# Performance work log

Hardware: AMD Instinct MI355X
Metric: run time of the kernel (lower is better)

Reference implementation:

```python
import jax, jax.numpy as jnp
import numpy as np
from functools import partial
from jax import lax

B, K, CLIP_DIM, SBERT_DIM, D_MODEL, R_RANK, ATTN_DIM, PMAX = 128, 1024, 768, 384, 256, 64, 256, 8
RHO = 0.35

def _normalize(x, axis=-1, eps=1e-12):
    return x / jnp.maximum(jnp.linalg.norm(x, axis=axis, keepdims=True), eps)

def _build_graph():
    rng = np.random.default_rng(0)
    pid = np.zeros((K, PMAX), np.int32)
    pm = np.zeros((K, PMAX), bool)
    for i in range(K - 1):  # node i's parents are in (i, K); root = K-1 has none
        n = int(rng.integers(1, PMAX + 1))
        n = min(n, K - 1 - i)
        cands = rng.choice(np.arange(i + 1, K), size=n, replace=False)
        pid[i, :n] = cands
        pm[i, :n] = True
    order = np.arange(K - 1, -1, -1, dtype=np.int32)  # parents before children
    return jnp.asarray(pid), jnp.asarray(pm), jnp.asarray(order)

def setup_inputs() -> dict:
    key = jax.random.key(0)
    ks = iter(jax.random.split(key, 32))
    r = lambda shape, s=0.02: jax.random.normal(next(ks), shape, jnp.float32) * s
    pid, pm, order = _build_graph()
    return {
        "t_clip": jax.random.normal(next(ks), (B, CLIP_DIM), jnp.float32),
        "v_clip": jax.random.normal(next(ks), (B, CLIP_DIM), jnp.float32),
        "concept_sbert": jax.random.normal(next(ks), (K, SBERT_DIM), jnp.float32),
        "Wt": r((CLIP_DIM, D_MODEL)), "bt": jnp.zeros((D_MODEL,)),
        "Wv": r((CLIP_DIM, D_MODEL)), "bv": jnp.zeros((D_MODEL,)),
        "Wc": r((SBERT_DIM, D_MODEL)), "bc": jnp.zeros((D_MODEL,)),
        "Wp1": r((3 * D_MODEL, 2 * D_MODEL)), "bp1": jnp.zeros((2 * D_MODEL,)),
        "Wp2": r((2 * D_MODEL, D_MODEL)), "bp2": jnp.zeros((D_MODEL,)),
        "Wm1": r((3 * D_MODEL, 2 * D_MODEL)), "bm1": jnp.zeros((2 * D_MODEL,)),
        "Wm2": r((2 * D_MODEL, D_MODEL)), "bm2": jnp.zeros((D_MODEL,)),
        "tau_logits": jnp.zeros((K,)),
        "U": r((D_MODEL, R_RANK)), "V": r((D_MODEL, R_RANK)),
        "Wg1": r((SBERT_DIM, R_RANK)), "bg1": jnp.zeros((R_RANK,)),
        "Wg2": r((R_RANK, R_RANK)), "bg2": jnp.zeros((R_RANK,)),
        "w_out": r((K, R_RANK)), "b_out": jnp.zeros((K,)),
        "concept_q": r((K, ATTN_DIM)),
        "parents_idx": pid, "parents_mask": pm, "order": order,
    }

def _forward(t_clip, v_clip, concept_sbert, Wt, bt, Wv, bv, Wc, bc,
             Wp1, bp1, Wp2, bp2, Wm1, bm1, Wm2, bm2, tau_logits,
             U, V, Wg1, bg1, Wg2, bg2, w_out, b_out, concept_q,
             parents_idx, parents_mask, order):
    gelu = partial(jax.nn.gelu, approximate=False)  # torch nn.GELU default = exact erf
    t = _normalize(t_clip) @ Wt + bt                 # [B, D]
    v = _normalize(v_clip) @ Wv + bv                 # [B, D]
    d = concept_sbert @ Wc + bc                      # [K, D]
    # x = [v, t, d] broadcast to [B, K, 3D]
    x = jnp.concatenate([
        jnp.broadcast_to(v[:, None, :], (t.shape[0], K, D_MODEL)),
        jnp.broadcast_to(t[:, None, :], (t.shape[0], K, D_MODEL)),
        jnp.broadcast_to(d[None, :, :], (t.shape[0], K, D_MODEL)),
    ], axis=-1)
    h_plus = gelu(x @ Wp1 + bp1) @ Wp2 + bp2
    h_minus = gelu(x @ Wm1 + bm1) @ Wm2 + bm2
    tau = jax.nn.sigmoid(tau_logits)[None, :, None]
    h = tau * h_plus + (1.0 - tau) * h_minus         # [B, K, D]
    u = jnp.einsum('bkd,dr->bkr', h, U)
    vv = jnp.einsum('bkd,dr->bkr', h, V)
    g = gelu(concept_sbert @ Wg1 + bg1) @ Wg2 + bg2  # [K, R]
    inter = u * vv * g[None, :, :]
    logits = jnp.einsum('bkr,kr->bk', inter, w_out) + b_out[None, :]
    p = jax.nn.sigmoid(logits)                        # [B, K]
    # --- top-down hierarchical attention + multiplicative aggregation ---
    q = _normalize(concept_q)                         # [K, A]
    def step(p_hat, node):
        par = parents_idx[node]                       # [P] int
        m = parents_mask[node]                        # [P] bool
        scores = jnp.where(m, q[par] @ q[node], -1e9)
        alpha = jax.nn.softmax(scores)                # [P]
        vals = p_hat[:, par]                          # [B, P] gather of parent probs
        prod = jnp.prod(jnp.where(m[None, :], alpha[None, :] * vals, 1.0), axis=-1)
        new = jnp.where(m.any(), RHO * p[:, node] + (1.0 - RHO) * prod, p_hat[:, node])
        return p_hat.at[:, node].set(new), None       # scatter write
    p_hat, _ = lax.scan(step, p, order)
    return p_hat

def reference(t_clip, v_clip, concept_sbert, Wt, bt, Wv, bv, Wc, bc,
              Wp1, bp1, Wp2, bp2, Wm1, bm1, Wm2, bm2, tau_logits,
              U, V, Wg1, bg1, Wg2, bg2, w_out, b_out, concept_q,
              parents_idx, parents_mask, order):
    return _forward(t_clip, v_clip, concept_sbert, Wt, bt, Wv, bv, Wc, bc,
                    Wp1, bp1, Wp2, bp2, Wm1, bm1, Wm2, bm2, tau_logits,
                    U, V, Wg1, bg1, Wg2, bg2, w_out, b_out, concept_q,
                    parents_idx, parents_mask, order)
```

## Files before the change

kernel.cpp:

```cpp
#include <hip/hip_runtime.h>
#include <math.h>

typedef __attribute__((ext_vector_type(8))) short short8;
typedef __attribute__((ext_vector_type(4))) float float4v;
typedef __attribute__((ext_vector_type(2))) float float2v;

struct P {
  const float *t_clip, *v_clip, *sbert;
  const float *Wt, *bt, *Wv, *bv, *Wc, *bc;
  const float *Wp1, *bp1, *Wp2, *bp2, *Wm1, *bm1, *Wm2, *bm2;
  const float *tau_logits, *U, *V, *Wg1, *bg1, *Wg2, *bg2, *w_out, *b_out, *concept_q;
  const int *pid;
  unsigned short *tvbf;
  unsigned short *sbbf;
  unsigned short *wtvB;
  unsigned short *wcB;
  unsigned short *wg1B;
  unsigned short *wg2B;
  unsigned short *w2bf;
  unsigned short *uvB;
  unsigned short *w1upP, *w1upM;
  unsigned short *w1lowP, *w1lowM;
  unsigned short *vtbf;
  unsigned short *dbf;
  unsigned short *ghbf;
  unsigned short *Ctp, *Ctm;
  unsigned short *Wpk, *Wmk;
  float *Ap, *Am;
  float *sBuf, *biasPM, *tau, *gw, *aprod;
  unsigned short *parS;
  int *sorted, *lvlStart, *nlev;
  float *pOut;
};

__device__ __forceinline__ unsigned short bf16ru(float f) {
    unsigned u = __float_as_uint(f);
    u += 0x7fffu + ((u >> 16) & 1u);
    return (unsigned short)(u >> 16);
}

__device__ __forceinline__ void glds16(const void* g, void* l) {
    __builtin_amdgcn_global_load_lds((const __attribute__((address_space(1))) unsigned int*)g,
                                     (__attribute__((address_space(3))) unsigned int*)l, 16, 0, 0);
}

__device__ __forceinline__ unsigned packpair(float2v a, unsigned c) {
    float2v cb;
    cb.x = __uint_as_float(c << 16);
    cb.y = __uint_as_float(c & 0xffff0000u);
    float2v x = a + cb;
    float2v t = x * x;
    float2v i = t * (-0.06649038f) + 0.39894228f;
    float2v p = x * i + 0.5f;
    float2v g = x * p;
    union { float2v f; unsigned u[2]; } gu; gu.f = g;
    return __builtin_amdgcn_perm(gu.u[1], gu.u[0], 0x07060302u);
}


__device__ void bconv_f(const float* __restrict__ srcRow0, unsigned short* __restrict__ dst,
                        int N, int K16, int kbase, char* smc) {
    unsigned short* wl = (unsigned short*)smc;
    int tid = threadIdx.x;
    int tot4 = 4 * N;
    for (int i4 = tid; i4 < tot4; i4 += 256) {
        float4 w = ((const float4*)srcRow0)[i4];
        ushort4 o;
        o.x = bf16ru(w.x); o.y = bf16ru(w.y); o.z = bf16ru(w.z); o.w = bf16ru(w.w);
        *(ushort4*)&wl[i4 * 4] = o;
    }
    __syncthreads();
    for (int i = tid; i < 2 * N; i += 256) {
        int kg = (i >= N) ? 1 : 0;
        int n = i - kg * N;
        int k0 = kbase + kg * 8;
        ushort4 o0, o1;
        o0.x = wl[(kg * 8 + 0) * N + n]; o0.y = wl[(kg * 8 + 1) * N + n];
        o0.z = wl[(kg * 8 + 2) * N + n]; o0.w = wl[(kg * 8 + 3) * N + n];
        o1.x = wl[(kg * 8 + 4) * N + n]; o1.y = wl[(kg * 8 + 5) * N + n];
        o1.z = wl[(kg * 8 + 6) * N + n]; o1.w = wl[(kg * 8 + 7) * N + n];
        size_t off = (size_t)(n >> 4) * K16 + (k0 >> 5) * 512 + ((k0 >> 3) & 3) * 128 + (n & 15) * 8;
        *(ushort4*)&dst[off]     = o0;
        *(ushort4*)&dst[off + 4] = o1;
    }
}

__device__ void aconv_f(const float* __restrict__ src, unsigned short* __restrict__ dst,
                        int r0, int K, int K16) {
    int tid = threadIdx.x;
    int Kq = K >> 2;
    for (int rl = 0; rl < 16; ++rl) {
        int row = r0 + rl;
        for (int i = tid; i < Kq; i += 256) {
            float4 w = ((const float4*)(src + (size_t)row * K))[i];
            ushort4 o;
            o.x = bf16ru(w.x); o.y = bf16ru(w.y); o.z = bf16ru(w.z); o.w = bf16ru(w.w);
            int k4 = i * 4;
            size_t off = (size_t)(row >> 4) * K16 + (k4 >> 5) * 512 + ((k4 >> 3) & 3) * 128
                       + (row & 15) * 8 + (k4 & 7);
            *(ushort4*)&dst[off] = o;
        }
    }
}

__device__ void tcv_f(const P& a, int rel) {
    int sel = rel & 1, r8 = rel >> 1;
    const float* X = sel ? a.t_clip : a.v_clip;
    unsigned short* dst = a.tvbf + sel * 98304;
    int tid = threadIdx.x;
    int rl = tid >> 5, l = tid & 31;
    int b = r8 * 8 + rl;
    const float4* src = (const float4*)(X + (size_t)b * 768);
    float ss = 0.f;
#pragma unroll
    for (int j = 0; j < 6; ++j) {
        int i4 = l + j * 32;
        float4 w = src[i4];
        ss += w.x * w.x + w.y * w.y + w.z * w.z + w.w * w.w;
        ushort4 o;
        o.x = bf16ru(w.x); o.y = bf16ru(w.y); o.z = bf16ru(w.z); o.w = bf16ru(w.w);
        int k4 = i4 * 4;
        size_t off = (size_t)(b >> 4) * 12288 + (k4 >> 5) * 512 + ((k4 >> 3) & 3) * 128
                   + (b & 15) * 8 + (k4 & 7);
        *(ushort4*)&dst[off] = o;
    }
#pragma unroll
    for (int mk = 16; mk; mk >>= 1) ss += __shfl_xor(ss, mk);
    if (l == 0) a.sBuf[sel * 128 + b] = 1.0f / fmaxf(sqrtf(ss), 1e-12f);
}

__device__ void uvconv_f(const P& a, int blk, char* smc) {
    unsigned short* wl = (unsigned short*)smc;
    int kbase = blk * 16;
    int tid = threadIdx.x;
    for (int i = tid; i < 2048; i += 256) {
        int kl = i >> 7, n = i & 127;
        float v = (n < 64) ? a.U[(size_t)(kbase + kl) * 64 + n]
                           : a.V[(size_t)(kbase + kl) * 64 + (n - 64)];
        wl[kl * 128 + n] = bf16ru(v);
    }
    __syncthreads();
    {
        int i = tid;
        int kg = i >> 7, n = i & 127;
        int k0 = kbase + kg * 8;
        ushort4 o0, o1;
        o0.x = wl[(kg * 8 + 0) * 128 + n]; o0.y = wl[(kg * 8 + 1) * 128 + n];
        o0.z = wl[(kg * 8 + 2) * 128 + n]; o0.w = wl[(kg * 8 + 3) * 128 + n];
        o1.x = wl[(kg * 8 + 4) * 128 + n]; o1.y = wl[(kg * 8 + 5) * 128 + n];
        o1.z = wl[(kg * 8 + 6) * 128 + n]; o1.w = wl[(kg * 8 + 7) * 128 + n];
        size_t off = (size_t)(n >> 4) * 4096 + (k0 >> 5) * 512 + ((k0 >> 3) & 3) * 128 + (n & 15) * 8;
        *(ushort4*)&a.uvB[off]     = o0;
        *(ushort4*)&a.uvB[off + 4] = o1;
    }
}

__device__ void biasPM_f(const P& a, int blk) {
    int tid = threadIdx.x;
    int o = blk * 32 + (tid >> 3), e = tid & 7;
    const float* bb = (o < 128) ? a.bp2 : a.bm2;
    int c = o & 127;
    const float* uv = (c < 64) ? (a.U + c) : (a.V + (c - 64));
    float acc = 0.f;
    for (int d = e * 32; d < e * 32 + 32; ++d)
        acc = fmaf(bb[d], uv[(size_t)d * 64], acc);
    acc += __shfl_xor(acc, 1);
    acc += __shfl_xor(acc, 2);
    acc += __shfl_xor(acc, 4);
    if (e == 0) a.biasPM[o] = acc;
}

__device__ void alpha_f(const P& a, int blk) {
    int t = threadIdx.x, wv = t >> 6, lane = t & 63;
    int node = blk * 4 + wv;
    int slot = lane >> 3, e = lane & 7;
    int par = a.pid[node * 8 + slot];
    const float4* qk = (const float4*)(a.concept_q + (size_t)node * 256);
    const float4* qp = (const float4*)(a.concept_q + (size_t)par * 256);
    float dq = 0, np = 0, ns = 0;
#pragma unroll
    for (int i = 0; i < 8; ++i) {
        float4 x = qp[e * 8 + i], y = qk[e * 8 + i];
        dq += x.x * y.x + x.y * y.y + x.z * y.z + x.w * y.w;
        np += x.x * x.x + x.y * x.y + x.z * x.z + x.w * x.w;
        ns += y.x * y.x + y.y * y.y + y.z * y.z + y.w * y.w;
    }
#pragma unroll
    for (int mk = 1; mk <= 4; mk <<= 1) {
        dq += __shfl_xor(dq, mk); np += __shfl_xor(np, mk); ns += __shfl_xor(ns, mk);
    }
    float score = dq / fmaxf(sqrtf(np) * sqrtf(ns), 1e-24f);
    float sc[8]; int pv[8];
#pragma unroll
    for (int s = 0; s < 8; ++s) { sc[s] = __shfl(score, s * 8); pv[s] = __shfl(par, s * 8); }
    float mx = -1e30f;
#pragma unroll
    for (int s = 0; s < 8; ++s) if (pv[s] != 0) mx = fmaxf(mx, sc[s]);
    float sum = 0.f;
#pragma unroll
    for (int s = 0; s < 8; ++s) sum += (pv[s] != 0) ? expf(sc[s] - mx) : 0.0f;
    float ap = 1.0f;
#pragma unroll
    for (int s = 0; s < 8; ++s) if (pv[s] != 0) ap *= expf(sc[s] - mx) / sum;
    if (lane == 0) a.aprod[node] = ap;
    if (e == 0) a.parS[node * 8 + slot] = (par != 0) ? (unsigned short)par : (unsigned short)1024;
}

__device__ void levels_f(const P& a, int* smemI) {
    volatile int* lvl = smemI;
    unsigned short* parL = (unsigned short*)(smemI + 1024);
    int* cnt  = smemI + 1024 + 4096;
    int* ofs  = smemI + 1024 + 4096 + 1024;
    int* ping = smemI + 1024 + 4096 + 2048;
    int* pong = ping + 256;
    int* mflag = pong + 256;
    int t = threadIdx.x;
    for (int i = t; i < 8192; i += 256) parL[i] = (unsigned short)a.pid[i];
    for (int i = t; i < 1024; i += 256) lvl[i] = 0;
    if (t == 0) mflag[1] = 0;
    __syncthreads();
    if (t < 64) {
        for (int c = 15; c >= 0; --c) {
            int n = c * 64 + t;
            ushort4 pA = *(const ushort4*)&parL[n * 8];
            ushort4 pB = *(const ushort4*)&parL[n * 8 + 4];
            for (;;) {
                int mx = -1;
                if (pA.x) mx = max(mx, lvl[pA.x]);
                if (pA.y) mx = max(mx, lvl[pA.y]);
                if (pA.z) mx = max(mx, lvl[pA.z]);
                if (pA.w) mx = max(mx, lvl[pA.w]);
                if (pB.x) mx = max(mx, lvl[pB.x]);
                if (pB.y) mx = max(mx, lvl[pB.y]);
                if (pB.z) mx = max(mx, lvl[pB.z]);
                if (pB.w) mx = max(mx, lvl[pB.w]);
                int nl = mx + 1;
                bool ch = (nl > lvl[n]);
                if (ch) lvl[n] = nl;
                if (__ballot(ch) == 0ULL) break;
            }
        }
    }
    __syncthreads();
    int lm = 0;
    for (int r = 0; r < 4; ++r) lm = max(lm, lvl[t * 4 + r]);
    atomicMax(&mflag[1], lm);
    for (int r = 0; r < 4; ++r) cnt[t * 4 + r] = 0;
    __syncthreads();
    for (int r = 0; r < 4; ++r) atomicAdd(&cnt[lvl[t * 4 + r]], 1);
    __syncthreads();
    int c0 = cnt[t * 4], c1 = cnt[t * 4 + 1], c2 = cnt[t * 4 + 2], c3 = cnt[t * 4 + 3];
    ping[t] = c0 + c1 + c2 + c3;
    __syncthreads();
    int* src = ping; int* dst = pong;
    for (int off = 1; off < 256; off <<= 1) {
        int v = src[t];
        if (t >= off) v += src[t - off];
        dst[t] = v;
        __syncthreads();
        int* tmp = src; src = dst; dst = tmp;
    }
    int excl = (t == 0) ? 0 : src[t - 1];
    ofs[t * 4] = excl; ofs[t * 4 + 1] = excl + c0;
    ofs[t * 4 + 2] = excl + c0 + c1; ofs[t * 4 + 3] = excl + c0 + c1 + c2;
#pragma unroll
    for (int r = 0; r < 4; ++r) a.lvlStart[t * 4 + r] = ofs[t * 4 + r];
    if (t == 0) { a.lvlStart[1024] = 1024; a.nlev[0] = mflag[1] + 1; }
    __syncthreads();
    for (int r = 0; r < 4; ++r) {
        int n = t * 4 + r;
        int pos = atomicAdd(&ofs[lvl[n]], 1);
        a.sorted[pos] = n;
    }
}

__global__ void __launch_bounds__(256) prep0_kernel(P a) {
    __shared__ int smem[7712];
    int bid = blockIdx.x;
    if (bid == 0) { levels_f(a, smem); return; }
    bid -= 1;
    if (bid < 96) {
        int mat = bid & 1, rb = bid >> 1;
        int r0 = rb * 16;
        const float* W1 = mat ? a.Wm1 : a.Wp1;
        if (r0 < 512) bconv_f(W1 + (size_t)r0 * 512, mat ? a.w1upM : a.w1upP, 512, 8192, r0, (char*)smem);
        else          bconv_f(W1 + (size_t)r0 * 512, mat ? a.w1lowM : a.w1lowP, 512, 4096, r0 - 512, (char*)smem);
        return;
    }
    bid -= 96;
    if (bid < 96) {
        int sel = bid & 1, ch = bid >> 1;
        bconv_f((sel ? a.Wt : a.Wv) + (size_t)ch * 16 * 256, a.wtvB + sel * 196608, 256, 12288, ch * 16, (char*)smem);
        return;
    }
    bid -= 96;
    if (bid < 24) { bconv_f(a.Wc + (size_t)bid * 16 * 256, a.wcB, 256, 6144, bid * 16, (char*)smem); return; }
    bid -= 24;
    if (bid < 24) { bconv_f(a.Wg1 + (size_t)bid * 16 * 64, a.wg1B, 64, 6144, bid * 16, (char*)smem); return; }
    bid -= 24;
    if (bid < 4) { bconv_f(a.Wg2 + (size_t)bid * 16 * 64, a.wg2B, 64, 1024, bid * 16, (char*)smem); return; }
    bid -= 4;
    if (bid < 64) {
        int mat = bid & 1, ch = bid >> 1;
        aconv_f(mat ? a.Wm2 : a.Wp2, a.w2bf + mat * 131072, ch * 16, 256, 4096);
        return;
    }
    bid -= 64;
    if (bid < 16) { uvconv_f(a, bid, (char*)smem); return; }
    bid -= 16;
    if (bid < 32) { tcv_f(a, bid); return; }
    bid -= 32;
    if (bid < 64) { aconv_f(a.sbert, a.sbbf, bid * 16, 384, 6144); return; }
    bid -= 64;
    if (bid < 256) { alpha_f(a, bid); return; }
    bid -= 256;
    if (bid < 8) { biasPM_f(a, bid); return; }
    bid -= 8;
    { int k = bid * 256 + threadIdx.x; a.tau[k] = 1.0f / (1.0f + expf(-a.tau_logits[k])); }
}

__device__ __forceinline__ void gemm64(const unsigned short* A, const unsigned short* B,
                                       int K16A, int K16B, int nsteps,
                                       float4v acc[4], int m, int quad) {
    const unsigned short* Ab = A + quad * 128 + m * 8;
    const unsigned short* Bb = B + quad * 128 + m * 8;
    for (int s = 0; s < nsteps; ++s) {
        short8 af = *(const short8*)(Ab + s * 512);
#pragma unroll
        for (int nt = 0; nt < 4; ++nt) {
            short8 bf = *(const short8*)(Bb + (size_t)nt * K16B + s * 512);
            acc[nt] = __builtin_amdgcn_mfma_f32_16x16x32_bf16(af, bf, acc[nt], 0, 0, 0);
        }
    }
}

__global__ void __launch_bounds__(256) prep1_kernel(P a) {
    int bid = blockIdx.x;
    int tid = threadIdx.x;
    int wv = tid >> 6, lane = tid & 63;
    int m = lane & 15, quad = lane >> 4;
    float4v acc[4];
#pragma unroll
    for (int i = 0; i < 4; ++i) acc[i] = (float4v)0.0f;

    if (bid < 16) {
        int sel = bid & 1, mt = (bid >> 1) & 1, ntile = bid >> 2;
        const unsigned short* A = a.tvbf + sel * 98304 + (size_t)(mt * 4 + wv) * 12288;
        const unsigned short* B = a.wtvB + sel * 196608 + (size_t)(ntile * 4) * 12288;
        gemm64(A, B, 12288, 12288, 24, acc, m, quad);
        const float* bias = sel ? a.bt : a.bv;
#pragma unroll
        for (int nt = 0; nt < 4; ++nt) {
            int col = ntile * 64 + nt * 16 + m;
            int vtcol = sel * 256 + col;
            float bb = bias[col];
#pragma unroll
            for (int r = 0; r < 4; ++r) {
                int row = mt * 64 + wv * 16 + quad * 4 + r;
                float val = acc[nt][r] * a.sBuf[sel * 128 + row] + bb;
                size_t off = (size_t)(row >> 4) * 8192 + (vtcol >> 5) * 512
                           + ((vtcol >> 3) & 3) * 128 + (row & 15) * 8 + (vtcol & 7);
                a.vtbf[off] = bf16ru(val);
            }
        }
        return;
    }
    bid -= 16;
    if (bid < 64) {
        int mt = bid & 15, ntile = bid >> 4;
        const unsigned short* A = a.sbbf + (size_t)(mt * 4 + wv) * 6144;
        const unsigned short* B = a.wcB + (size_t)(ntile * 4) * 6144;
        gemm64(A, B, 6144, 6144, 12, acc, m, quad);
#pragma unroll
        for (int nt = 0; nt < 4; ++nt) {
            int col = ntile * 64 + nt * 16 + m;
            float bb = a.bc[col];
#pragma unroll
            for (int r = 0; r < 4; ++r) {
                int row = mt * 64 + wv * 16 + quad * 4 + r;
                size_t off = (size_t)(row >> 4) * 4096 + (col >> 5) * 512
                           + ((col >> 3) & 3) * 128 + (row & 15) * 8 + (col & 7);
                a.dbf[off] = bf16ru(acc[nt][r] + bb);
            }
        }
        return;
    }
    bid -= 64;
    if (bid < 16) {
        int mt = bid;
        const unsigned short* A = a.sbbf + (size_t)(mt * 4 + wv) * 6144;
        gemm64(A, a.wg1B, 6144, 6144, 12, acc, m, quad);
#pragma unroll
        for (int nt = 0; nt < 4; ++nt) {
            int col = nt * 16 + m;
            float bb = a.bg1[col];
#pragma unroll
            for (int r = 0; r < 4; ++r) {
                int row = mt * 64 + wv * 16 + quad * 4 + r;
                float x = acc[nt][r] + bb;
                float g = 0.5f * x * (1.0f + erff(x * 0.7071067811865475f));
                size_t off = (size_t)(row >> 4) * 1024 + (col >> 5) * 512
                           + ((col >> 3) & 3) * 128 + (row & 15) * 8 + (col & 7);
                a.ghbf[off] = bf16ru(g);
            }
        }
        return;
    }
    bid -= 16;
    {
        int mat = bid & 1, mt = (bid >> 1) & 7, ntile = bid >> 4;
        const unsigned short* A = a.w2bf + mat * 131072 + (size_t)(mt * 4 + wv) * 4096;
        const unsigned short* B = a.uvB + (size_t)(ntile * 4) * 4096;
        gemm64(A, B, 4096, 4096, 8, acc, m, quad);
        unsigned short* outP = mat ? a.Wmk : a.Wpk;
#pragma unroll
        for (int nt = 0; nt < 4; ++nt) {
            int c = ntile * 64 + nt * 16 + m;
#pragma unroll
            for (int r = 0; r < 4; ++r) {
                int j = mt * 64 + wv * 16 + quad * 4 + r;
                size_t o = (size_t)(j >> 5) * 4096 + (c >> 4) * 512 + ((j >> 3) & 3) * 128
                         + (c & 15) * 8 + (j & 7);
                outP[o] = bf16ru(acc[nt][r]);
            }
        }
    }
}

__global__ void __launch_bounds__(256) prep2_kernel(P a) {
    int bid = blockIdx.x;
    int tid = threadIdx.x;
    int wv = tid >> 6, lane = tid & 63;
    int m = lane & 15, quad = lane >> 4;
    if (bid < 256) {
        int mat = bid & 1, mt = (bid >> 1) & 15, ntile = bid >> 5;
        const unsigned short* A = a.dbf + (size_t)(mt * 4 + wv) * 4096 + quad * 128 + m * 8;
        const unsigned short* B = (mat ? a.w1lowM : a.w1lowP) + (size_t)quad * 128 + m * 8;
        unsigned short* Ct = mat ? a.Ctm : a.Ctp;
        float4v acc[4];
#pragma unroll
        for (int i = 0; i < 4; ++i) acc[i] = (float4v)0.0f;
        for (int s = 0; s < 8; ++s) {
            short8 af = *(const short8*)(A + s * 512);
#pragma unroll
            for (int nt = 0; nt < 4; ++nt) {
                short8 bf = *(const short8*)(B + (size_t)(ntile * 4 + nt) * 4096 + s * 512);
                acc[nt] = __builtin_amdgcn_mfma_f32_16x16x32_bf16(af, bf, acc[nt], 0, 0, 0);
            }
        }
        int rowg = mt * 4 + wv;
        int rl = quad * 4;
#pragma unroll
        for (int nt = 0; nt < 4; ++nt) {
            int j = ntile * 64 + nt * 16 + m;
            size_t base = (size_t)rowg * 8192 + (j >> 5) * 512 + ((j >> 3) & 3) * 128 + (j & 7);
#pragma unroll
            for (int rr = 0; rr < 4; ++rr)
                Ct[base + (rl + rr) * 8] = bf16ru(acc[nt][rr]);
        }
        return;
    }
    bid -= 256;
    if (bid < 32) {
        int mat = bid & 1, mt = (bid >> 1) & 1, ntile = bid >> 2;
        const unsigned short* A = a.vtbf + (size_t)(mt * 4 + wv) * 8192 + quad * 128 + m * 8;
        const unsigned short* B = (mat ? a.w1upM : a.w1upP) + (size_t)quad * 128 + m * 8;
        const float* bias = mat ? a.bm1 : a.bp1;
        float* out = mat ? a.Am : a.Ap;
        float4v acc[4];
#pragma unroll
        for (int i = 0; i < 4; ++i) acc[i] = (float4v)0.0f;
        for (int s = 0; s < 16; ++s) {
            short8 af = *(const short8*)(A + s * 512);
#pragma unroll
            for (int nt = 0; nt < 4; ++nt) {
                short8 bf = *(const short8*)(B + (size_t)(ntile * 4 + nt) * 8192 + s * 512);
                acc[nt] = __builtin_amdgcn_mfma_f32_16x16x32_bf16(af, bf, acc[nt], 0, 0, 0);
            }
        }
        int b0r = mt * 64 + wv * 16 + quad * 4;
#pragma unroll
        for (int nt = 0; nt < 4; ++nt) {
            int j = ntile * 64 + nt * 16 + m;
            float bb = bias[j];
#pragma unroll
            for (int rr = 0; rr < 4; ++rr)
                out[(size_t)(b0r + rr) * 512 + j] = acc[nt][rr] + bb;
        }
        return;
    }
    bid -= 32;
    {
        int mt = bid;
        const unsigned short* A = a.ghbf + (size_t)(mt * 4 + wv) * 1024 + quad * 128 + m * 8;
        const unsigned short* B = a.wg2B + (size_t)quad * 128 + m * 8;
        float4v acc[4];
#pragma unroll
        for (int i = 0; i < 4; ++i) acc[i] = (float4v)0.0f;
        for (int s = 0; s < 2; ++s) {
            short8 af = *(const short8*)(A + s * 512);
#pragma unroll
            for (int nt = 0; nt < 4; ++nt) {
                short8 bf = *(const short8*)(B + (size_t)nt * 1024 + s * 512);
                acc[nt] = __builtin_amdgcn_mfma_f32_16x16x32_bf16(af, bf, acc[nt], 0, 0, 0);
            }
        }
#pragma unroll
        for (int nt = 0; nt < 4; ++nt) {
            int col = nt * 16 + m;
            float bb = a.bg2[col];
#pragma unroll
            for (int r = 0; r < 4; ++r) {
                int k = mt * 64 + wv * 16 + quad * 4 + r;
                a.gw[(size_t)k * 64 + col] = (acc[nt][r] + bb) * a.w_out[(size_t)k * 64 + col];
            }
        }
    }
}

__global__ void __launch_bounds__(512, 2) main_kernel(P a) {
    __shared__ float apL[4096];
    __shared__ char wbuf[2][16384];
    int tid = threadIdx.x;
    int wv2 = tid >> 6, lane = tid & 63;
    int mat = wv2 >> 2, sub = wv2 & 3;
    int m = lane & 15, quad = lane >> 4;
    int b0 = (blockIdx.x >> 4) * 4;
    int k0 = (blockIdx.x & 15) << 6;

    for (int i = tid; i < 1024; i += 512) {
        int arr = i >> 7, off = i & 127;
        const float* src = ((arr >> 2) ? a.Am : a.Ap) + (size_t)(b0 + (arr & 3)) * 512;
        ((float4*)apL)[i] = ((const float4*)src)[off];
    }

    const char* wg = ((wv2 < 4) ? (const char*)a.Wpk : (const char*)a.Wmk)
                   + (wv2 & 3) * 2048 + lane * 16;
    char* wl0 = &wbuf[0][wv2 * 2048];
    char* wl1 = &wbuf[1][wv2 * 2048];

    const unsigned short* Ct = mat ? a.Ctm : a.Ctp;
    const float* aL = apL + mat * 2048;
    int kt = (k0 >> 4) + sub;
    const char* ctB = (const char*)Ct + (size_t)kt * 16384 + quad * 256 + m * 16;

    float4v acc[4][8];
#pragma unroll
    for (int b = 0; b < 4; ++b)
#pragma unroll
        for (int i = 0; i < 8; ++i) acc[b][i] = (float4v)0.0f;

    glds16(wg, wl0);
    glds16(wg + 1024, wl0 + 1024);
    uint4 crN = *(const uint4*)(ctB);
    __syncthreads();

    for (int n = 0; n < 16; ++n) {
        if (n < 15) {
            char* dst = ((n + 1) & 1) ? wl1 : wl0;
            glds16(wg + (n + 1) * 8192, dst);
            glds16(wg + (n + 1) * 8192 + 1024, dst + 1024);
        }
        uint4 cr = crN;
        if (n < 15) crN = *(const uint4*)(ctB + (n + 1) * 1024);
        union { uint4 u; short8 s; } fa[4];
        const float* aj = aL + n * 32 + quad * 8;
#pragma unroll
        for (int b = 0; b < 4; ++b) {
            float4v x0 = *(const float4v*)(aj + b * 512);
            float4v x1 = *(const float4v*)(aj + b * 512 + 4);
            float2v v;
            v.x = x0[0]; v.y = x0[1]; fa[b].u.x = packpair(v, cr.x);
            v.x = x0[2]; v.y = x0[3]; fa[b].u.y = packpair(v, cr.y);
            v.x = x1[0]; v.y = x1[1]; fa[b].u.z = packpair(v, cr.z);
            v.x = x1[2]; v.y = x1[3]; fa[b].u.w = packpair(v, cr.w);
        }
        const char* wB = &wbuf[n & 1][0] + mat * 8192 + quad * 256 + m * 16;
#pragma unroll
        for (int nt = 0; nt < 8; ++nt) {
            short8 wf = *(const short8*)(wB + nt * 1024);
            acc[0][nt] = __builtin_amdgcn_mfma_f32_16x16x32_bf16(fa[0].s, wf, acc[0][nt], 0, 0, 0);
            acc[1][nt] = __builtin_amdgcn_mfma_f32_16x16x32_bf16(fa[1].s, wf, acc[1][nt], 0, 0, 0);
            acc[2][nt] = __builtin_amdgcn_mfma_f32_16x16x32_bf16(fa[2].s, wf, acc[2][nt], 0, 0, 0);
            acc[3][nt] = __builtin_amdgcn_mfma_f32_16x16x32_bf16(fa[3].s, wf, acc[3][nt], 0, 0, 0);
        }
        __syncthreads();
    }

    float* xbuf = (float*)wbuf;
    int kk[4]; float tv[4];
#pragma unroll
    for (int r = 0; r < 4; ++r) { kk[r] = k0 + sub * 16 + quad * 4 + r; tv[r] = a.tau[kk[r]]; }
    float lsum[4][4] = {};
#pragma unroll
    for (int t4 = 0; t4 < 4; ++t4) {
        __syncthreads();
        if (mat == 1) {
#pragma unroll
            for (int b = 0; b < 4; ++b) {
                int slot = (sub * 4 + b) * 64 + lane;
#pragma unroll
                for (int r = 0; r < 4; ++r) {
                    xbuf[r * 1024 + slot]       = acc[b][t4][r];
                    xbuf[(r + 4) * 1024 + slot] = acc[b][t4 + 4][r];
                }
            }
        }
        __syncthreads();
        if (mat == 0) {
            int cU = t4 * 16 + m, cV = cU + 64;
            float bPu = a.biasPM[cU], bMu = a.biasPM[128 + cU];
            float bPv = a.biasPM[cV], bMv = a.biasPM[128 + cV];
#pragma unroll
            for (int b = 0; b < 4; ++b) {
                int slot = (sub * 4 + b) * 64 + lane;
#pragma unroll
                for (int r = 0; r < 4; ++r) {
                    float g = a.gw[(size_t)kk[r] * 64 + cU];
                    float u  = tv[r] * (acc[b][t4][r] + bPu)
                             + (1.0f - tv[r]) * (xbuf[r * 1024 + slot] + bMu);
                    float vx = tv[r] * (acc[b][t4 + 4][r] + bPv)
                             + (1.0f - tv[r]) * (xbuf[(r + 4) * 1024 + slot] + bMv);
                    lsum[b][r] = fmaf(u * vx, g, lsum[b][r]);
                }
            }
        }
    }
    if (mat == 0) {
#pragma unroll
        for (int r = 0; r < 4; ++r) {
            float bo = a.b_out[kk[r]];
#pragma unroll
            for (int b = 0; b < 4; ++b) {
                float s = lsum[b][r];
                s += __shfl_xor(s, 1); s += __shfl_xor(s, 2); s += __shfl_xor(s, 4); s += __shfl_xor(s, 8);
                if (m == 0)
                    a.pOut[(size_t)(b0 + b) * 1024 + kk[r]] = 1.0f / (1.0f + expf(-(s + bo)));
            }
        }
    }
}

#define PH_STRIDE 1056
__global__ void __launch_bounds__(256) scan_kernel(P a) {
    __shared__ float ph[4 * PH_STRIDE];
    __shared__ float aprodL[1024];
    __shared__ unsigned short parL[8192];
    __shared__ short sortedL[1024];
    __shared__ int lvlStartL[1025];
    int t = threadIdx.x;
    int b0 = blockIdx.x * 4;
    for (int i = t; i < 1024; i += 256) ((uint4*)parL)[i] = ((const uint4*)a.parS)[i];
    for (int i = t; i < 1024; i += 256) {
        aprodL[i] = a.aprod[i];
        sortedL[i] = (short)a.sorted[i];
        lvlStartL[i] = a.lvlStart[i];
    }
    if (t == 0) lvlStartL[1024] = 1024;
    for (int i = t; i < 4096; i += 256) {
        int bb = i >> 10, k = i & 1023;
        ph[bb * PH_STRIDE + k] = a.pOut[(size_t)(b0 + bb) * 1024 + k];
    }
    if (t < 4) ph[t * PH_STRIDE + 1024] = 1.0f;
    __syncthreads();
    int nlev = a.nlev[0];
    int w = t >> 6, lane = t & 63;
    float* myph = ph + w * PH_STRIDE;
    for (int L = 1; L < nlev; ++L) {
        int s0 = lvlStartL[L], s1 = lvlStartL[L + 1];
        for (int i = s0 + lane; i < s1; i += 64) {
            int node = sortedL[i];
            ushort4 pA = *(const ushort4*)&parL[node * 8];
            ushort4 pB = *(const ushort4*)&parL[node * 8 + 4];
            float prod = aprodL[node];
            prod *= myph[pA.x] * myph[pA.y];
            prod *= myph[pA.z] * myph[pA.w];
            prod *= myph[pB.x] * myph[pB.y];
            prod *= myph[pB.z] * myph[pB.w];
            myph[node] = fmaf(0.35f, myph[node], 0.65f * prod);
        }
    }
    __syncthreads();
    for (int i = t; i < 4096; i += 256) {
        int bb = i >> 10, k = i & 1023;
        a.pOut[(size_t)(b0 + bb) * 1024 + k] = ph[bb * PH_STRIDE + k];
    }
}

extern "C" void kernel_launch(void* const* d_in, const int* in_sizes, int n_in,
                              void* d_out, int out_size, void* d_ws, size_t ws_size,
                              hipStream_t stream) {
    P a;
    a.t_clip = (const float*)d_in[0];
    a.v_clip = (const float*)d_in[1];
    a.sbert  = (const float*)d_in[2];
    a.Wt  = (const float*)d_in[3];  a.bt  = (const float*)d_in[4];
    a.Wv  = (const float*)d_in[5];  a.bv  = (const float*)d_in[6];
    a.Wc  = (const float*)d_in[7];  a.bc  = (const float*)d_in[8];
    a.Wp1 = (const float*)d_in[9];  a.bp1 = (const float*)d_in[10];
    a.Wp2 = (const float*)d_in[11]; a.bp2 = (const float*)d_in[12];
    a.Wm1 = (const float*)d_in[13]; a.bm1 = (const float*)d_in[14];
    a.Wm2 = (const float*)d_in[15]; a.bm2 = (const float*)d_in[16];
    a.tau_logits = (const float*)d_in[17];
    a.U   = (const float*)d_in[18]; a.V   = (const float*)d_in[19];
    a.Wg1 = (const float*)d_in[20]; a.bg1 = (const float*)d_in[21];
    a.Wg2 = (const float*)d_in[22]; a.bg2 = (const float*)d_in[23];
    a.w_out = (const float*)d_in[24]; a.b_out = (const float*)d_in[25];
    a.concept_q = (const float*)d_in[26];
    a.pid = (const int*)d_in[27];

    char* w = (char*)d_ws;
    a.Ctp  = (unsigned short*)(w + 0);
    a.Ctm  = (unsigned short*)(w + 1048576);
    a.tvbf = (unsigned short*)(w + 0);
    a.sbbf = (unsigned short*)(w + 393216);
    a.wtvB = (unsigned short*)(w + 1179648);
    a.wcB  = (unsigned short*)(w + 1966080);
    a.w1upP  = (unsigned short*)(w + 2162688);
    a.w1upM  = (unsigned short*)(w + 2686976);
    a.w1lowP = (unsigned short*)(w + 3211264);
    a.w1lowM = (unsigned short*)(w + 3473408);
    a.wg1B   = (unsigned short*)(w + 3735552);
    a.wg2B   = (unsigned short*)(w + 3784704);
    a.w2bf   = (unsigned short*)(w + 3792896);
    a.uvB    = (unsigned short*)(w + 4317184);
    a.vtbf   = (unsigned short*)(w + 4382720);
    a.dbf    = (unsigned short*)(w + 4513792);
    a.ghbf   = (unsigned short*)(w + 5038080);
    a.Wpk    = (unsigned short*)(w + 5169152);
    a.Wmk    = (unsigned short*)(w + 5300224);
    a.Ap     = (float*)(w + 5431296);
    a.Am     = (float*)(w + 5693440);
    a.biasPM = (float*)(w + 5955584);
    a.tau    = (float*)(w + 5956608);
    a.gw     = (float*)(w + 5960704);
    a.sBuf   = (float*)(w + 6222848);
    a.parS   = (unsigned short*)(w + 6223872);
    a.aprod  = (float*)(w + 6240256);
    a.sorted = (int*)(w + 6244352);
    a.lvlStart = (int*)(w + 6248448);
    a.nlev     = (int*)(w + 6252672);
    a.pOut = (float*)d_out;

    prep0_kernel<<<689, 256, 0, stream>>>(a);
    prep1_kernel<<<128, 256, 0, stream>>>(a);
    prep2_kernel<<<304, 256, 0, stream>>>(a);
    main_kernel<<<512, 512, 0, stream>>>(a);
    scan_kernel<<<32, 256, 0, stream>>>(a);
}
```

Before: 246.1 us.

## Merge prep kernels with grid barriers and fold scan into main kernel tail

Fuses the three prep kernels into one persistent launch of 689 blocks separated by atomic grid-wide barriers, and appends the scan stage to main_kernel: the last 32 blocks to arrive at an atomic counter wait for all blocks, then each runs the level-ordered scan for 4 batch rows. This removes three kernel launch boundaries and their drain/fill gaps. It relies on all 689 prep blocks being co-resident, otherwise the barrier deadlocks. It also adds spin-waiting and a memset launch, and the scan tail runs on only 32 blocks while the rest of the grid has exited.

```diff
diff --git a/kernel.cpp b/kernel.cpp
--- a/kernel.cpp
+++ b/kernel.cpp
@@ -44,6 +44,18 @@
                                      (__attribute__((address_space(3))) unsigned int*)l, 16, 0, 0);
 }
 
+__device__ __forceinline__ void gridbar(unsigned* cnt, unsigned nblk) {
+    __threadfence();
+    __syncthreads();
+    if (threadIdx.x == 0) {
+        __hip_atomic_fetch_add(cnt, 1u, __ATOMIC_RELEASE, __HIP_MEMORY_SCOPE_AGENT);
+        while (__hip_atomic_load(cnt, __ATOMIC_ACQUIRE, __HIP_MEMORY_SCOPE_AGENT) < nblk)
+            __builtin_amdgcn_s_sleep(2);
+    }
+    __syncthreads();
+    __threadfence();
+}
+
 __device__ __forceinline__ unsigned packpair(float2v a, unsigned c) {
     float2v cb;
     cb.x = __uint_as_float(c << 16);
@@ -274,9 +286,7 @@
     }
 }
 
-__global__ void __launch_bounds__(256) prep0_kernel(P a) {
-    __shared__ int smem[7712];
-    int bid = blockIdx.x;
+__device__ void prep0_body(const P& a, int bid, int* smem) {
     if (bid == 0) { levels_f(a, smem); return; }
     bid -= 1;
     if (bid < 96) {
@@ -320,7 +330,7 @@
 }
 
 __device__ __forceinline__ void gemm64(const unsigned short* A, const unsigned short* B,
-                                       int K16A, int K16B, int nsteps,
+                                       int K16B, int nsteps,
                                        float4v acc[4], int m, int quad) {
     const unsigned short* Ab = A + quad * 128 + m * 8;
     const unsigned short* Bb = B + quad * 128 + m * 8;
@@ -334,8 +344,7 @@
     }
 }
 
-__global__ void __launch_bounds__(256) prep1_kernel(P a) {
-    int bid = blockIdx.x;
+__device__ void prep1_body(const P& a, int bid) {
     int tid = threadIdx.x;
     int wv = tid >> 6, lane = tid & 63;
     int m = lane & 15, quad = lane >> 4;
@@ -347,7 +356,7 @@
         int sel = bid & 1, mt = (bid >> 1) & 1, ntile = bid >> 2;
         const unsigned short* A = a.tvbf + sel * 98304 + (size_t)(mt * 4 + wv) * 12288;
         const unsigned short* B = a.wtvB + sel * 196608 + (size_t)(ntile * 4) * 12288;
-        gemm64(A, B, 12288, 12288, 24, acc, m, quad);
+        gemm64(A, B, 12288, 24, acc, m, quad);
         const float* bias = sel ? a.bt : a.bv;
 #pragma unroll
         for (int nt = 0; nt < 4; ++nt) {
@@ -370,7 +379,7 @@
         int mt = bid & 15, ntile = bid >> 4;
         const unsigned short* A = a.sbbf + (size_t)(mt * 4 + wv) * 6144;
         const unsigned short* B = a.wcB + (size_t)(ntile * 4) * 6144;
-        gemm64(A, B, 6144, 6144, 12, acc, m, quad);
+        gemm64(A, B, 6144, 12, acc, m, quad);
 #pragma unroll
         for (int nt = 0; nt < 4; ++nt) {
             int col = ntile * 64 + nt * 16 + m;
@@ -389,7 +398,7 @@
     if (bid < 16) {
         int mt = bid;
         const unsigned short* A = a.sbbf + (size_t)(mt * 4 + wv) * 6144;
-        gemm64(A, a.wg1B, 6144, 6144, 12, acc, m, quad);
+        gemm64(A, a.wg1B, 6144, 12, acc, m, quad);
 #pragma unroll
         for (int nt = 0; nt < 4; ++nt) {
             int col = nt * 16 + m;
@@ -411,7 +420,7 @@
         int mat = bid & 1, mt = (bid >> 1) & 7, ntile = bid >> 4;
         const unsigned short* A = a.w2bf + mat * 131072 + (size_t)(mt * 4 + wv) * 4096;
         const unsigned short* B = a.uvB + (size_t)(ntile * 4) * 4096;
-        gemm64(A, B, 4096, 4096, 8, acc, m, quad);
+        gemm64(A, B, 4096, 8, acc, m, quad);
         unsigned short* outP = mat ? a.Wmk : a.Wpk;
 #pragma unroll
         for (int nt = 0; nt < 4; ++nt) {
@@ -427,8 +436,7 @@
     }
 }
 
-__global__ void __launch_bounds__(256) prep2_kernel(P a) {
-    int bid = blockIdx.x;
+__device__ void prep2_body(const P& a, int bid) {
     int tid = threadIdx.x;
     int wv = tid >> 6, lane = tid & 63;
     int m = lane & 15, quad = lane >> 4;
@@ -518,9 +526,20 @@
     }
 }
 
-__global__ void __launch_bounds__(512, 2) main_kernel(P a) {
-    __shared__ float apL[4096];
-    __shared__ char wbuf[2][16384];
+__global__ void __launch_bounds__(256, 4) prep_all_kernel(P a, unsigned* bar) {
+    __shared__ int smem[7712];
+    prep0_body(a, blockIdx.x, smem);
+    gridbar(&bar[0], 689u);
+    if (blockIdx.x < 128) prep1_body(a, blockIdx.x);
+    gridbar(&bar[1], 689u);
+    if (blockIdx.x < 304) prep2_body(a, blockIdx.x);
+}
+
+__global__ void __launch_bounds__(512, 2) main_kernel(P a, unsigned* barM) {
+    __shared__ char shm[49152];
+    __shared__ unsigned arrivalS;
+    float* apL = (float*)shm;
+    char* wbufB = shm + 16384;
     int tid = threadIdx.x;
     int wv2 = tid >> 6, lane = tid & 63;
     int mat = wv2 >> 2, sub = wv2 & 3;
@@ -536,8 +555,8 @@
 
     const char* wg = ((wv2 < 4) ? (const char*)a.Wpk : (const char*)a.Wmk)
                    + (wv2 & 3) * 2048 + lane * 16;
-    char* wl0 = &wbuf[0][wv2 * 2048];
-    char* wl1 = &wbuf[1][wv2 * 2048];
+    char* wl0 = wbufB + wv2 * 2048;
+    char* wl1 = wbufB + 16384 + wv2 * 2048;
 
     const unsigned short* Ct = mat ? a.Ctm : a.Ctp;
     const float* aL = apL + mat * 2048;
@@ -575,7 +594,7 @@
             v.x = x1[0]; v.y = x1[1]; fa[b].u.z = packpair(v, cr.z);
             v.x = x1[2]; v.y = x1[3]; fa[b].u.w = packpair(v, cr.w);
         }
-        const char* wB = &wbuf[n & 1][0] + mat * 8192 + quad * 256 + m * 16;
+        const char* wB = wbufB + (n & 1) * 16384 + mat * 8192 + quad * 256 + m * 16;
 #pragma unroll
         for (int nt = 0; nt < 8; ++nt) {
             short8 wf = *(const short8*)(wB + nt * 1024);
@@ -587,7 +606,7 @@
         __syncthreads();
     }
 
-    float* xbuf = (float*)wbuf;
+    float* xbuf = (float*)wbufB;
     int kk[4]; float tv[4];
 #pragma unroll
     for (int r = 0; r < 4; ++r) { kk[r] = k0 + sub * 16 + quad * 4 + r; tv[r] = a.tau[kk[r]]; }
@@ -639,51 +658,65 @@
             }
         }
     }
-}
-
-#define PH_STRIDE 1056
-__global__ void __launch_bounds__(256) scan_kernel(P a) {
-    __shared__ float ph[4 * PH_STRIDE];
-    __shared__ float aprodL[1024];
-    __shared__ unsigned short parL[8192];
-    __shared__ short sortedL[1024];
-    __shared__ int lvlStartL[1025];
-    int t = threadIdx.x;
-    int b0 = blockIdx.x * 4;
-    for (int i = t; i < 1024; i += 256) ((uint4*)parL)[i] = ((const uint4*)a.parS)[i];
-    for (int i = t; i < 1024; i += 256) {
-        aprodL[i] = a.aprod[i];
-        sortedL[i] = (short)a.sorted[i];
-        lvlStartL[i] = a.lvlStart[i];
-    }
-    if (t == 0) lvlStartL[1024] = 1024;
-    for (int i = t; i < 4096; i += 256) {
-        int bb = i >> 10, k = i & 1023;
-        ph[bb * PH_STRIDE + k] = a.pOut[(size_t)(b0 + bb) * 1024 + k];
-    }
-    if (t < 4) ph[t * PH_STRIDE + 1024] = 1.0f;
-    __syncthreads();
-    int nlev = a.nlev[0];
-    int w = t >> 6, lane = t & 63;
-    float* myph = ph + w * PH_STRIDE;
-    for (int L = 1; L < nlev; ++L) {
-        int s0 = lvlStartL[L], s1 = lvlStartL[L + 1];
-        for (int i = s0 + lane; i < s1; i += 64) {
-            int node = sortedL[i];
-            ushort4 pA = *(const ushort4*)&parL[node * 8];
-            ushort4 pB = *(const ushort4*)&parL[node * 8 + 4];
-            float prod = aprodL[node];
-            prod *= myph[pA.x] * myph[pA.y];
-            prod *= myph[pA.z] * myph[pA.w];
-            prod *= myph[pB.x] * myph[pB.y];
-            prod *= myph[pB.z] * myph[pB.w];
-            myph[node] = fmaf(0.35f, myph[node], 0.65f * prod);
-        }
-    }
-    __syncthreads();
-    for (int i = t; i < 4096; i += 256) {
-        int bb = i >> 10, k = i & 1023;
-        a.pOut[(size_t)(b0 + bb) * 1024 + k] = ph[bb * PH_STRIDE + k];
+
+    __threadfence();
+    __syncthreads();
+    if (tid == 0)
+        arrivalS = __hip_atomic_fetch_add(barM, 1u, __ATOMIC_RELEASE, __HIP_MEMORY_SCOPE_AGENT);
+    __syncthreads();
+    unsigned arr = arrivalS;
+    if (arr < 480u) return;
+    if (tid == 0) {
+        while (__hip_atomic_load(barM, __ATOMIC_ACQUIRE, __HIP_MEMORY_SCOPE_AGENT) < 512u)
+            __builtin_amdgcn_s_sleep(2);
+    }
+    __syncthreads();
+    __threadfence();
+    {
+        int task = (int)(arr - 480u);
+        int b0s = task * 4;
+        float* ph = (float*)shm;
+        float* aprodL = (float*)(shm + 16896);
+        unsigned short* parL = (unsigned short*)(shm + 20992);
+        short* sortedL = (short*)(shm + 37376);
+        int* lvlStartL = (int*)(shm + 39424);
+        for (int i = tid; i < 1024; i += 512) ((uint4*)parL)[i] = ((const uint4*)a.parS)[i];
+        for (int i = tid; i < 1024; i += 512) {
+            aprodL[i] = a.aprod[i];
+            sortedL[i] = (short)a.sorted[i];
+            lvlStartL[i] = a.lvlStart[i];
+        }
+        if (tid == 0) lvlStartL[1024] = 1024;
+        for (int i = tid; i < 4096; i += 512) {
+            int bb = i >> 10, k = i & 1023;
+            ph[bb * 1056 + k] = a.pOut[(size_t)(b0s + bb) * 1024 + k];
+        }
+        if (tid < 4) ph[tid * 1056 + 1024] = 1.0f;
+        __syncthreads();
+        int nlev = a.nlev[0];
+        int w = tid >> 6;
+        if (w < 4) {
+            float* myph = ph + w * 1056;
+            for (int L = 1; L < nlev; ++L) {
+                int s0 = lvlStartL[L], s1 = lvlStartL[L + 1];
+                for (int i = s0 + lane; i < s1; i += 64) {
+                    int node = sortedL[i];
+                    ushort4 pA = *(const ushort4*)&parL[node * 8];
+                    ushort4 pB = *(const ushort4*)&parL[node * 8 + 4];
+                    float prod = aprodL[node];
+                    prod *= myph[pA.x] * myph[pA.y];
+                    prod *= myph[pA.z] * myph[pA.w];
+                    prod *= myph[pB.x] * myph[pB.y];
+                    prod *= myph[pB.z] * myph[pB.w];
+                    myph[node] = fmaf(0.35f, myph[node], 0.65f * prod);
+                }
+            }
+        }
+        __syncthreads();
+        for (int i = tid; i < 4096; i += 512) {
+            int bb = i >> 10, k = i & 1023;
+            a.pOut[(size_t)(b0s + bb) * 1024 + k] = ph[bb * 1056 + k];
+        }
     }
 }
 
@@ -742,9 +775,8 @@
     a.nlev     = (int*)(w + 6252672);
     a.pOut = (float*)d_out;
 
-    prep0_kernel<<<689, 256, 0, stream>>>(a);
-    prep1_kernel<<<128, 256, 0, stream>>>(a);
-    prep2_kernel<<<304, 256, 0, stream>>>(a);
-    main_kernel<<<512, 512, 0, stream>>>(a);
-    scan_kernel<<<32, 256, 0, stream>>>(a);
-}
+    unsigned* bar = (unsigned*)(w + 6256640);
+    hipMemsetAsync(bar, 0, 64, stream);
+    prep_all_kernel<<<689, 256, 0, stream>>>(a, bar);
+    main_kernel<<<512, 512, 0, stream>>>(a, bar + 2);
+}
```

Result: slower. 760.5 us (+209.1%).
